# Optimization experiments

Hardware: AMD Instinct MI355X
Metric: run time of the kernel (lower is better)

## Reference

```python
import jax, jax.numpy as jnp
import numpy as np

TOKENS = 16384
DIM = 7168
N_EXPERTS = 256
N_GROUPS = 8          # n_expert_groups
TOPK_GROUPS = 4       # n_limited_groups
TOPK = 8              # n_activated_experts
ROUTE_SCALE = 2.5


def setup_inputs() -> dict:
    key = jax.random.key(0)
    k1, k2, k3 = jax.random.split(key, 3)
    x = jax.random.normal(k1, (TOKENS, DIM), dtype=jnp.float32)
    weight = jax.random.normal(k2, (N_EXPERTS, DIM), dtype=jnp.float32) * 0.02
    bias = jax.random.normal(k3, (N_EXPERTS,), dtype=jnp.float32) * 0.02
    return {"x": x, "weight": weight, "bias": bias}


def reference(x, weight, bias):
    T = x.shape[0]
    # router GEMM: [T, D] @ [D, E] -> [T, E]
    logits = jnp.einsum('td,ed->te', x, weight)
    scores = jax.nn.sigmoid(logits)            # score_func == 'sigmoid'
    original_scores = scores
    scores = scores + bias                     # bias path (dim == 7168)
    # group-limited routing: [T, G, E/G]
    sg = scores.reshape(T, N_GROUPS, -1)
    # bias is not None -> group score = sum of top-2 per group
    group_scores = jax.lax.top_k(sg, 2)[0].sum(axis=-1)          # [T, G]
    gidx = jax.lax.top_k(group_scores, TOPK_GROUPS)[1]           # [T, topk_groups]
    mask = jnp.zeros((T, N_GROUPS), dtype=scores.dtype)
    mask = mask.at[jnp.arange(T)[:, None], gidx].set(1.0)        # scatter mask
    scores_masked = (sg * mask[:, :, None]).reshape(T, -1)       # [T, E]
    idx = jax.lax.top_k(scores_masked, TOPK)[1]                  # [T, topk]
    w = jnp.take_along_axis(original_scores, idx, axis=1)        # gather
    w = w / w.sum(axis=-1, keepdims=True)                        # sigmoid norm
    w = w * ROUTE_SCALE
    return w.astype(x.dtype), idx
```

## Files before the change

### kernel.cpp

```cpp
#include <hip/hip_runtime.h>
#include <float.h>
#include <math.h>

#define TOKENS 16384
#define DIM    7168
#define NEXP   256
#define BM     32
#define BK     32
#define NCHUNK (DIM / BK)
#define ROUTE_SCALE 2.5
#define TAU      6e-6f
#define WSCALE   1024.0f
#define WUNSCALE 0.0009765625f
#define FIXCAP   8192

typedef _Float16 half8  __attribute__((ext_vector_type(8)));
typedef _Float16 half4v __attribute__((ext_vector_type(4)));
typedef float    f32x4  __attribute__((ext_vector_type(4)));

#define WPLANE 1835008

__device__ __forceinline__ _Float16 hi16(float f) { return (_Float16)f; }
__device__ __forceinline__ _Float16 lo16(float f) {
    _Float16 h = (_Float16)f;
    return (_Float16)(f - (float)h);
}

__global__ __launch_bounds__(256)
void conv_w(const float* __restrict__ W, _Float16* __restrict__ Wh, _Float16* __restrict__ Wl,
            int* __restrict__ cnt) {
    if (blockIdx.x == 0 && threadIdx.x == 0) *cnt = 0;
    int i = blockIdx.x * 256 + threadIdx.x;
    int f = i * 4;
    int e = f / DIM;
    int k = f - e * DIM;
    float4 v = ((const float4*)W)[i];
    v.x *= WSCALE; v.y *= WSCALE; v.z *= WSCALE; v.w *= WSCALE;
    half4v h, l;
    h[0] = hi16(v.x); l[0] = lo16(v.x);
    h[1] = hi16(v.y); l[1] = lo16(v.y);
    h[2] = hi16(v.z); l[2] = lo16(v.z);
    h[3] = hi16(v.w); l[3] = lo16(v.w);
    int o = ((k >> 5) << 13) + (e << 5) + (k & 31);
    *(half4v*)(Wh + o) = h;
    *(half4v*)(Wl + o) = l;
}

#define MFMA16(a, b, c) __builtin_amdgcn_mfma_f32_16x16x32_f16(a, b, c, 0, 0, 0)

#define VWAIT(n) do { \
    asm volatile("s_waitcnt vmcnt(" #n ")" ::: "memory"); \
    __builtin_amdgcn_sched_barrier(0); \
} while (0)

#define ISSUE_WS(c, S) do { \
    const _Float16* _p = wph0 + (size_t)(c) * 8192; \
    const _Float16* _q = wpl0 + (size_t)(c) * 8192; \
    asm volatile("global_load_dwordx4 %0, %1, off"             : "=&v"(S##h0) : "v"(_p)); \
    asm volatile("global_load_dwordx4 %0, %1, off offset:1024" : "=&v"(S##h1) : "v"(_p)); \
    asm volatile("global_load_dwordx4 %0, %1, off"             : "=&v"(S##l0) : "v"(_q)); \
    asm volatile("global_load_dwordx4 %0, %1, off offset:1024" : "=&v"(S##l1) : "v"(_q)); \
} while (0)

#define ISSUE_XP(gg, XA, XB) do { \
    const float* _px = xsrc + (size_t)(gg) * 64; \
    asm volatile("global_load_dwordx4 %0, %1, off"           : "=&v"(XA) : "v"(_px)); \
    asm volatile("global_load_dwordx4 %0, %1, off offset:16" : "=&v"(XB) : "v"(_px)); \
} while (0)

#define COMPUTE(ABP, BH0, BH1, BL0, BL1) do { \
    const _Float16* _ab = (ABP); \
    half8 ah0 = *(const half8*)(_ab + abase0); \
    half8 ah1 = *(const half8*)(_ab + abase1); \
    half8 al0 = *(const half8*)(_ab + 1024 + abase0); \
    half8 al1 = *(const half8*)(_ab + 1024 + abase1); \
    __builtin_amdgcn_s_setprio(1); \
    acc00 = MFMA16(ah0, BH0, acc00); acc00 = MFMA16(ah0, BL0, acc00); acc00 = MFMA16(al0, BH0, acc00); \
    acc01 = MFMA16(ah0, BH1, acc01); acc01 = MFMA16(ah0, BL1, acc01); acc01 = MFMA16(al0, BH1, acc01); \
    acc10 = MFMA16(ah1, BH0, acc10); acc10 = MFMA16(ah1, BL0, acc10); acc10 = MFMA16(al1, BH0, acc10); \
    acc11 = MFMA16(ah1, BH1, acc11); acc11 = MFMA16(ah1, BL1, acc11); acc11 = MFMA16(al1, BH1, acc11); \
    __builtin_amdgcn_s_setprio(0); \
} while (0)

#define COMPUTE_S(ABP, S) COMPUTE(ABP, S##h0, S##h1, S##l0, S##l1)

#define DUMPF() do { \
    accf00 += acc00; acc00 = (f32x4)(0.0f); \
    accf01 += acc01; acc01 = (f32x4)(0.0f); \
    accf10 += acc10; acc10 = (f32x4)(0.0f); \
    accf11 += acc11; acc11 = (f32x4)(0.0f); \
} while (0)

#define CONVERT_WRITE_XP(dstbuf, XA, XB) do { \
    half8 h8, l8; \
    const float v[8] = {XA.x, XA.y, XA.z, XA.w, XB.x, XB.y, XB.z, XB.w}; \
    _Pragma("unroll") \
    for (int e = 0; e < 8; ++e) { h8[e] = hi16(v[e]); l8[e] = lo16(v[e]); } \
    _Float16* d = hb + (dstbuf) * 4096 + xdst; \
    *(half8*)(d)        = h8; \
    *(half8*)(d + 1024) = l8; \
} while (0)

__global__ __launch_bounds__(256, 4)
void gate_main(const float* __restrict__ X, const _Float16* __restrict__ Wh,
               const _Float16* __restrict__ Wl, float* __restrict__ LG) {
    __shared__ _Float16 hb[8192];

    const int tid  = threadIdx.x;
    const int lane = tid & 63;
    const int ns   = tid >> 6;
    const int bid  = blockIdx.x;
    const int eh   = (bid >> 2) & 1;
    const int mt   = (bid >> 3) * 4 + (bid & 3);
    const int m0   = mt * BM;
    const int fr   = lane & 15;
    const int fk   = lane >> 4;

    const int xcc = tid >> 7;
    const int xr  = (tid >> 2) & 31;
    const int xs  = tid & 3;
    const float* xsrc = X + (size_t)(m0 + xr) * DIM + xcc * 32 + xs * 8;
    const int xdst = xcc * 2048 + xr * 32 + ((xs ^ ((xr >> 1) & 3)) << 3);

    const int row0 = fr;
    const int row1 = fr + 16;
    const int abase0 = row0 * 32 + ((fk ^ ((row0 >> 1) & 3)) << 3);
    const int abase1 = row1 * 32 + ((fk ^ ((row1 >> 1) & 3)) << 3);

    const int wro = ((eh * 128 + ns * 32 + fr) << 5) + fk * 8;
    const _Float16* wph0 = Wh + wro;
    const _Float16* wpl0 = Wl + wro;

    f32x4 acc00 = {}, acc01 = {}, acc10 = {}, acc11 = {};
    f32x4 accf00 = {}, accf01 = {}, accf10 = {}, accf11 = {};
    half8 S0h0, S0h1, S0l0, S0l1;
    half8 S1h0, S1h1, S1l0, S1l1;
    half8 S2h0, S2h1, S2l0, S2l1;
    half8 S3h0, S3h1, S3l0, S3l1;
    float4 xa, xb;
    float4 xc, xd;

    {
        float4 pa = *(const float4*)(xsrc);
        float4 pb = *(const float4*)(xsrc + 4);
        half8 h8, l8;
        const float v[8] = {pa.x, pa.y, pa.z, pa.w, pb.x, pb.y, pb.z, pb.w};
        #pragma unroll
        for (int e = 0; e < 8; ++e) { h8[e] = hi16(v[e]); l8[e] = lo16(v[e]); }
        *(half8*)(hb + xdst)        = h8;
        *(half8*)(hb + xdst + 1024) = l8;
    }
    asm volatile("s_waitcnt vmcnt(0) lgkmcnt(0)" ::: "memory");
    __builtin_amdgcn_sched_barrier(0);
    ISSUE_XP(1, xc, xd);
    ISSUE_WS(0, S0);
    ISSUE_WS(1, S1);
    __builtin_amdgcn_s_barrier();

    for (int k = 0; k < 55; ++k) {
        const int c4 = k * 4;
        VWAIT(4); ISSUE_XP(2 * k + 2, xa, xb); ISSUE_WS(c4 + 2, S2); COMPUTE_S(hb,        S0);
        VWAIT(6); ISSUE_WS(c4 + 3, S3);                              COMPUTE_S(hb + 2048, S1);
        CONVERT_WRITE_XP(1, xc, xd);
        asm volatile("s_waitcnt lgkmcnt(0)" ::: "memory");
        __builtin_amdgcn_s_barrier();
        VWAIT(4); ISSUE_XP(2 * k + 3, xc, xd); ISSUE_WS(c4 + 4, S0); COMPUTE_S(hb + 4096, S2);
        VWAIT(6); ISSUE_WS(c4 + 5, S1);                              COMPUTE_S(hb + 6144, S3);
        if ((k & 3) == 3) DUMPF();
        CONVERT_WRITE_XP(0, xa, xb);
        asm volatile("s_waitcnt lgkmcnt(0)" ::: "memory");
        __builtin_amdgcn_s_barrier();
    }
    VWAIT(4); ISSUE_WS(222, S2); COMPUTE_S(hb,        S0);
    VWAIT(4); ISSUE_WS(223, S3); COMPUTE_S(hb + 2048, S1);
    CONVERT_WRITE_XP(1, xc, xd);
    asm volatile("s_waitcnt lgkmcnt(0)" ::: "memory");
    __builtin_amdgcn_s_barrier();
    VWAIT(4); COMPUTE_S(hb + 4096, S2);
    VWAIT(0); COMPUTE_S(hb + 6144, S3);
    DUMPF();

    {
        f32x4 af[2][2] = {{accf00, accf01}, {accf10, accf11}};
        #pragma unroll
        for (int m = 0; m < 2; ++m)
            #pragma unroll
            for (int n = 0; n < 2; ++n)
                #pragma unroll
                for (int r = 0; r < 4; ++r) {
                    int t = m0 + m * 16 + fk * 4 + r;
                    int e = eh * 128 + ns * 32 + n * 16 + fr;
                    LG[(size_t)t * 256 + e] = af[m][n][r] * WUNSCALE;
                }
    }
}

__global__ __launch_bounds__(1024)
void gate_route(const float* __restrict__ LG, const float* __restrict__ Bp,
                float* __restrict__ outw, float* __restrict__ outi,
                int* __restrict__ cnt, int* __restrict__ list) {
    const int lane = threadIdx.x & 63;
    const int wv   = threadIdx.x >> 6;
    const int nw   = gridDim.x * 16;
    const int e0   = lane * 4;

    const float4 b4 = ((const float4*)Bp)[lane];

    for (int t = blockIdx.x * 16 + wv; t < TOKENS; t += nw) {
        float4 v4 = ((const float4*)LG)[(size_t)t * 64 + lane];
        const float s0 = 1.0f / (1.0f + expf(-v4.x));
        const float s1 = 1.0f / (1.0f + expf(-v4.y));
        const float s2 = 1.0f / (1.0f + expf(-v4.z));
        const float s3 = 1.0f / (1.0f + expf(-v4.w));
        const float c0 = s0 + b4.x, c1 = s1 + b4.y, c2 = s2 + b4.z, c3 = s3 + b4.w;

        float m1 = -FLT_MAX, m2 = -FLT_MAX;
        m2 = fmaxf(m2, fminf(m1, c0)); m1 = fmaxf(m1, c0);
        m2 = fmaxf(m2, fminf(m1, c1)); m1 = fmaxf(m1, c1);
        m2 = fmaxf(m2, fminf(m1, c2)); m1 = fmaxf(m1, c2);
        m2 = fmaxf(m2, fminf(m1, c3)); m1 = fmaxf(m1, c3);
        #pragma unroll
        for (int m = 1; m < 8; m <<= 1) {
            float o1 = __shfl_xor(m1, m);
            float o2 = __shfl_xor(m2, m);
            float hi = fmaxf(m1, o1);
            float lo = fmaxf(fminf(m1, o1), fmaxf(m2, o2));
            m1 = hi; m2 = lo;
        }
        const float gsl = m1 + m2;
        float gs[8];
        #pragma unroll
        for (int j = 0; j < 8; ++j) gs[j] = __shfl(gsl, j * 8);

        unsigned sel = 0;
        #pragma unroll
        for (int r = 0; r < 4; ++r) {
            float best = -FLT_MAX; int bg = 0;
            #pragma unroll
            for (int g = 0; g < 8; ++g) {
                int ok = (((sel >> g) & 1) == 0) & (gs[g] > best);
                best = ok ? gs[g] : best;
                bg   = ok ? g : bg;
            }
            sel |= 1u << bg;
        }
        float selmin = FLT_MAX, unselmax = -FLT_MAX;
        #pragma unroll
        for (int g = 0; g < 8; ++g) {
            int s = (sel >> g) & 1;
            selmin   = s ? fminf(selmin, gs[g])   : selmin;
            unselmax = s ? unselmax : fmaxf(unselmax, gs[g]);
        }
        bool flag = (selmin - unselmax) < (2.0f * TAU);

        const int gsel = (sel >> (lane >> 3)) & 1;
        const float z0 = gsel ? c0 : 0.0f;
        const float z1 = gsel ? c1 : 0.0f;
        const float z2 = gsel ? c2 : 0.0f;
        const float z3 = gsel ? c3 : 0.0f;

        float pv = FLT_MAX; int pe = -1;
        float wv8[8]; int ie8[8]; float wsum = 0.f;
        #pragma unroll
        for (int j = 0; j < 9; ++j) {
            float best = -FLT_MAX; int be = 0;
            {
                int af0 = (z0 < pv) | ((z0 == pv) & (e0     > pe));
                int tk0 = af0 & (z0 > best); best = tk0 ? z0 : best; be = tk0 ? e0     : be;
                int af1 = (z1 < pv) | ((z1 == pv) & (e0 + 1 > pe));
                int tk1 = af1 & (z1 > best); best = tk1 ? z1 : best; be = tk1 ? e0 + 1 : be;
                int af2 = (z2 < pv) | ((z2 == pv) & (e0 + 2 > pe));
                int tk2 = af2 & (z2 > best); best = tk2 ? z2 : best; be = tk2 ? e0 + 2 : be;
                int af3 = (z3 < pv) | ((z3 == pv) & (e0 + 3 > pe));
                int tk3 = af3 & (z3 > best); best = tk3 ? z3 : best; be = tk3 ? e0 + 3 : be;
            }
            #pragma unroll
            for (int m = 1; m < 64; m <<= 1) {
                float ov = __shfl_xor(best, m);
                int   oe = __shfl_xor(be, m);
                int take = (ov > best) | ((ov == best) & (oe < be));
                best = take ? ov : best;
                be   = take ? oe : be;
            }
            if (j > 0) flag = flag || ((pv - best) < TAU);
            if (j < 8) {
                const int ol = be >> 2, oi = be & 3;
                float w0 = __shfl(s0, ol), w1 = __shfl(s1, ol);
                float w2 = __shfl(s2, ol), w3 = __shfl(s3, ol);
                float ow = (oi == 0) ? w0 : (oi == 1) ? w1 : (oi == 2) ? w2 : w3;
                wv8[j] = ow; ie8[j] = be; wsum += ow;
            }
            pv = best; pe = be;
        }

        if (lane == 0) {
            if (flag) {
                int slot = atomicAdd(cnt, 1);
                list[slot] = t;
            }
            float scale = (float)ROUTE_SCALE / wsum;
            #pragma unroll
            for (int j = 0; j < 8; ++j) {
                outw[(size_t)t * 8 + j] = wv8[j] * scale;
                outi[(size_t)t * 8 + j] = (float)ie8[j];
            }
        }
    }
}

__global__ __launch_bounds__(256)
void gate_fix_dot(const float* __restrict__ X, const float* __restrict__ W,
                  const int* __restrict__ cnt, const int* __restrict__ list,
                  double* __restrict__ sig) {
    __shared__ float wlds[4 * DIM];
    const int tid  = threadIdx.x;
    const int lane = tid & 63;
    const int wv   = tid >> 6;
    const int eb   = blockIdx.x >> 2;
    const int tb   = blockIdx.x & 3;
    const int e    = eb * 4 + wv;
    int n = *cnt; if (n > FIXCAP) n = FIXCAP;

    for (int i = tid; i < DIM; i += 256)
        ((float4*)wlds)[i] = ((const float4*)(W + (size_t)eb * 4 * DIM))[i];
    __syncthreads();

    const float* wrow = wlds + wv * DIM;
    for (int li = tb; li < n; li += 8) {
        const int t0  = list[li];
        const int li1 = li + 4;
        const bool v1 = (li1 < n);
        const int t1  = v1 ? list[li1] : t0;
        const float* xr0 = X + (size_t)t0 * DIM;
        const float* xr1 = X + (size_t)t1 * DIM;
        double a0 = 0, a1 = 0, a2 = 0, a3 = 0;
        double b0 = 0, b1 = 0, b2 = 0, b3 = 0;
        for (int kk = 0; kk < DIM / 256; ++kk) {
            const int k = kk * 256 + lane * 4;
            float4 w4 = *(const float4*)(wrow + k);
            float4 x4 = *(const float4*)(xr0 + k);
            float4 y4 = *(const float4*)(xr1 + k);
            a0 = fma((double)x4.x, (double)w4.x, a0);
            a1 = fma((double)x4.y, (double)w4.y, a1);
            a2 = fma((double)x4.z, (double)w4.z, a2);
            a3 = fma((double)x4.w, (double)w4.w, a3);
            b0 = fma((double)y4.x, (double)w4.x, b0);
            b1 = fma((double)y4.y, (double)w4.y, b1);
            b2 = fma((double)y4.z, (double)w4.z, b2);
            b3 = fma((double)y4.w, (double)w4.w, b3);
        }
        double da = (a0 + a1) + (a2 + a3);
        double db = (b0 + b1) + (b2 + b3);
        #pragma unroll
        for (int m = 1; m < 64; m <<= 1) {
            da += __shfl_xor(da, m);
            db += __shfl_xor(db, m);
        }
        if (lane == 0) {
            sig[(size_t)li * 256 + e] = 1.0 / (1.0 + exp(-da));
            if (v1) sig[(size_t)li1 * 256 + e] = 1.0 / (1.0 + exp(-db));
        }
    }
}

__global__ __launch_bounds__(256)
void gate_fix_route(const float* __restrict__ Bp, float* __restrict__ outw,
                    float* __restrict__ outi, const int* __restrict__ cnt,
                    const int* __restrict__ list, const double* __restrict__ sig) {
    const int lane = threadIdx.x & 63;
    const int wv   = threadIdx.x >> 6;
    const int nw   = gridDim.x * 4;
    const int e0   = lane * 4;
    int n = *cnt; if (n > FIXCAP) n = FIXCAP;

    const float4 bf = ((const float4*)Bp)[lane];
    const double q0 = (double)bf.x, q1 = (double)bf.y, q2 = (double)bf.z, q3 = (double)bf.w;

    for (int li = blockIdx.x * 4 + wv; li < n; li += nw) {
        const int t = list[li];
        const double2 sa = ((const double2*)(sig + (size_t)li * 256))[lane * 2];
        const double2 sb = ((const double2*)(sig + (size_t)li * 256))[lane * 2 + 1];
        const double s0 = sa.x, s1 = sa.y, s2 = sb.x, s3 = sb.y;
        const double c0 = s0 + q0, c1 = s1 + q1, c2 = s2 + q2, c3 = s3 + q3;

        double m1 = -DBL_MAX, m2 = -DBL_MAX;
        m2 = fmax(m2, fmin(m1, c0)); m1 = fmax(m1, c0);
        m2 = fmax(m2, fmin(m1, c1)); m1 = fmax(m1, c1);
        m2 = fmax(m2, fmin(m1, c2)); m1 = fmax(m1, c2);
        m2 = fmax(m2, fmin(m1, c3)); m1 = fmax(m1, c3);
        #pragma unroll
        for (int m = 1; m < 8; m <<= 1) {
            double o1 = __shfl_xor(m1, m);
            double o2 = __shfl_xor(m2, m);
            double hi = fmax(m1, o1);
            double lo = fmax(fmin(m1, o1), fmax(m2, o2));
            m1 = hi; m2 = lo;
        }
        const double gsl = m1 + m2;
        double gs[8];
        #pragma unroll
        for (int j = 0; j < 8; ++j) gs[j] = __shfl(gsl, j * 8);

        unsigned sel = 0;
        #pragma unroll
        for (int r = 0; r < 4; ++r) {
            double best = -DBL_MAX; int bg = 0;
            #pragma unroll
            for (int g = 0; g < 8; ++g) {
                int ok = (((sel >> g) & 1) == 0) & (gs[g] > best);
                best = ok ? gs[g] : best;
                bg   = ok ? g : bg;
            }
            sel |= 1u << bg;
        }
        const int gsel = (sel >> (lane >> 3)) & 1;
        const double z0 = gsel ? c0 : 0.0;
        const double z1 = gsel ? c1 : 0.0;
        const double z2 = gsel ? c2 : 0.0;
        const double z3 = gsel ? c3 : 0.0;

        double pv = DBL_MAX; int pe = -1;
        double wv8[8]; int ie8[8]; double wsum = 0.0;
        #pragma unroll
        for (int j = 0; j < 8; ++j) {
            double best = -DBL_MAX; int be = 0;
            {
                int af0 = (z0 < pv) | ((z0 == pv) & (e0     > pe));
                int tk0 = af0 & (z0 > best); best = tk0 ? z0 : best; be = tk0 ? e0     : be;
                int af1 = (z1 < pv) | ((z1 == pv) & (e0 + 1 > pe));
                int tk1 = af1 & (z1 > best); best = tk1 ? z1 : best; be = tk1 ? e0 + 1 : be;
                int af2 = (z2 < pv) | ((z2 == pv) & (e0 + 2 > pe));
                int tk2 = af2 & (z2 > best); best = tk2 ? z2 : best; be = tk2 ? e0 + 2 : be;
                int af3 = (z3 < pv) | ((z3 == pv) & (e0 + 3 > pe));
                int tk3 = af3 & (z3 > best); best = tk3 ? z3 : best; be = tk3 ? e0 + 3 : be;
            }
            #pragma unroll
            for (int m = 1; m < 64; m <<= 1) {
                double ov = __shfl_xor(best, m);
                int    oe = __shfl_xor(be, m);
                int take = (ov > best) | ((ov == best) & (oe < be));
                best = take ? ov : best;
                be   = take ? oe : be;
            }
            {
                const int ol = be >> 2, oi = be & 3;
                double w0 = __shfl(s0, ol), w1 = __shfl(s1, ol);
                double w2 = __shfl(s2, ol), w3 = __shfl(s3, ol);
                double ow = (oi == 0) ? w0 : (oi == 1) ? w1 : (oi == 2) ? w2 : w3;
                wv8[j] = ow; ie8[j] = be; wsum += ow;
            }
            pv = best; pe = be;
        }
        if (lane == 0) {
            #pragma unroll
            for (int j = 0; j < 8; ++j) {
                outw[(size_t)t * 8 + j] = (float)((wv8[j] / wsum) * ROUTE_SCALE);
                outi[(size_t)t * 8 + j] = (float)ie8[j];
            }
        }
    }
}

extern "C" void kernel_launch(void* const* d_in, const int* in_sizes, int n_in,
                              void* d_out, int out_size, void* d_ws, size_t ws_size,
                              hipStream_t stream) {
    const float* X  = (const float*)d_in[0];
    const float* W  = (const float*)d_in[1];
    const float* Bp = (const float*)d_in[2];
    float* outw = (float*)d_out;
    float* outi = (float*)d_out + (size_t)TOKENS * 8;

    _Float16* Wh = (_Float16*)d_ws;
    _Float16* Wl = Wh + WPLANE;
    int* cnt  = (int*)(Wl + WPLANE);
    int* list = (int*)((char*)cnt + 16);
    float* LG = (float*)(list + TOKENS);
    double* sig = (double*)LG;

    conv_w        <<<dim3(WPLANE / 1024), dim3(256),  0, stream>>>(W, Wh, Wl, cnt);
    gate_main     <<<dim3(1024),          dim3(256),  0, stream>>>(X, Wh, Wl, LG);
    gate_route    <<<dim3(256),           dim3(1024), 0, stream>>>(LG, Bp, outw, outi, cnt, list);
    gate_fix_dot  <<<dim3(256),           dim3(256),  0, stream>>>(X, W, cnt, list, sig);
    gate_fix_route<<<dim3(64),            dim3(256),  0, stream>>>(Bp, outw, outi, cnt, list, sig);
}
```

Baseline: 454.2 us.

## Halve per-block expert tile to 64 and double grid for higher occupancy

Each block now computes a 32-token by 64-expert tile with one 16-wide expert fragment per wave, halving weight register staging and accumulators. The grid doubles to 2048 blocks and launch bounds target 6 waves per SIMD to improve latency hiding. In exchange, each token tile's X data is loaded and split into fp16 halves by four blocks instead of two. Each LDS A-fragment read now feeds half as many MFMAs.

```diff
diff --git a/kernel.cpp b/kernel.cpp
--- a/kernel.cpp
+++ b/kernel.cpp
@@ -53,13 +53,11 @@
     __builtin_amdgcn_sched_barrier(0); \
 } while (0)
 
-#define ISSUE_WS(c, S) do { \
+#define ISSUE_W2(c, H, L) do { \
     const _Float16* _p = wph0 + (size_t)(c) * 8192; \
     const _Float16* _q = wpl0 + (size_t)(c) * 8192; \
-    asm volatile("global_load_dwordx4 %0, %1, off"             : "=&v"(S##h0) : "v"(_p)); \
-    asm volatile("global_load_dwordx4 %0, %1, off offset:1024" : "=&v"(S##h1) : "v"(_p)); \
-    asm volatile("global_load_dwordx4 %0, %1, off"             : "=&v"(S##l0) : "v"(_q)); \
-    asm volatile("global_load_dwordx4 %0, %1, off offset:1024" : "=&v"(S##l1) : "v"(_q)); \
+    asm volatile("global_load_dwordx4 %0, %1, off" : "=&v"(H) : "v"(_p)); \
+    asm volatile("global_load_dwordx4 %0, %1, off" : "=&v"(L) : "v"(_q)); \
 } while (0)
 
 #define ISSUE_XP(gg, XA, XB) do { \
@@ -68,27 +66,21 @@
     asm volatile("global_load_dwordx4 %0, %1, off offset:16" : "=&v"(XB) : "v"(_px)); \
 } while (0)
 
-#define COMPUTE(ABP, BH0, BH1, BL0, BL1) do { \
+#define COMPUTE2(ABP, BH, BL) do { \
     const _Float16* _ab = (ABP); \
     half8 ah0 = *(const half8*)(_ab + abase0); \
     half8 ah1 = *(const half8*)(_ab + abase1); \
     half8 al0 = *(const half8*)(_ab + 1024 + abase0); \
     half8 al1 = *(const half8*)(_ab + 1024 + abase1); \
     __builtin_amdgcn_s_setprio(1); \
-    acc00 = MFMA16(ah0, BH0, acc00); acc00 = MFMA16(ah0, BL0, acc00); acc00 = MFMA16(al0, BH0, acc00); \
-    acc01 = MFMA16(ah0, BH1, acc01); acc01 = MFMA16(ah0, BL1, acc01); acc01 = MFMA16(al0, BH1, acc01); \
-    acc10 = MFMA16(ah1, BH0, acc10); acc10 = MFMA16(ah1, BL0, acc10); acc10 = MFMA16(al1, BH0, acc10); \
-    acc11 = MFMA16(ah1, BH1, acc11); acc11 = MFMA16(ah1, BL1, acc11); acc11 = MFMA16(al1, BH1, acc11); \
+    acc0 = MFMA16(ah0, BH, acc0); acc0 = MFMA16(ah0, BL, acc0); acc0 = MFMA16(al0, BH, acc0); \
+    acc1 = MFMA16(ah1, BH, acc1); acc1 = MFMA16(ah1, BL, acc1); acc1 = MFMA16(al1, BH, acc1); \
     __builtin_amdgcn_s_setprio(0); \
 } while (0)
 
-#define COMPUTE_S(ABP, S) COMPUTE(ABP, S##h0, S##h1, S##l0, S##l1)
-
 #define DUMPF() do { \
-    accf00 += acc00; acc00 = (f32x4)(0.0f); \
-    accf01 += acc01; acc01 = (f32x4)(0.0f); \
-    accf10 += acc10; acc10 = (f32x4)(0.0f); \
-    accf11 += acc11; acc11 = (f32x4)(0.0f); \
+    accf0 += acc0; acc0 = (f32x4)(0.0f); \
+    accf1 += acc1; acc1 = (f32x4)(0.0f); \
 } while (0)
 
 #define CONVERT_WRITE_XP(dstbuf, XA, XB) do { \
@@ -101,7 +93,7 @@
     *(half8*)(d + 1024) = l8; \
 } while (0)
 
-__global__ __launch_bounds__(256, 4)
+__global__ __launch_bounds__(256, 6)
 void gate_main(const float* __restrict__ X, const _Float16* __restrict__ Wh,
                const _Float16* __restrict__ Wl, float* __restrict__ LG) {
     __shared__ _Float16 hb[8192];
@@ -110,8 +102,8 @@
     const int lane = tid & 63;
     const int ns   = tid >> 6;
     const int bid  = blockIdx.x;
-    const int eh   = (bid >> 2) & 1;
-    const int mt   = (bid >> 3) * 4 + (bid & 3);
+    const int eq   = (bid >> 1) & 3;
+    const int mt   = (bid >> 3) * 2 + (bid & 1);
     const int m0   = mt * BM;
     const int fr   = lane & 15;
     const int fk   = lane >> 4;
@@ -127,16 +119,13 @@
     const int abase0 = row0 * 32 + ((fk ^ ((row0 >> 1) & 3)) << 3);
     const int abase1 = row1 * 32 + ((fk ^ ((row1 >> 1) & 3)) << 3);
 
-    const int wro = ((eh * 128 + ns * 32 + fr) << 5) + fk * 8;
+    const int wro = ((eq * 64 + ns * 16 + fr) << 5) + fk * 8;
     const _Float16* wph0 = Wh + wro;
     const _Float16* wpl0 = Wl + wro;
 
-    f32x4 acc00 = {}, acc01 = {}, acc10 = {}, acc11 = {};
-    f32x4 accf00 = {}, accf01 = {}, accf10 = {}, accf11 = {};
-    half8 S0h0, S0h1, S0l0, S0l1;
-    half8 S1h0, S1h1, S1l0, S1l1;
-    half8 S2h0, S2h1, S2l0, S2l1;
-    half8 S3h0, S3h1, S3l0, S3l1;
+    f32x4 acc0 = {}, acc1 = {};
+    f32x4 accf0 = {}, accf1 = {};
+    half8 S0h, S0l, S1h, S1l, S2h, S2l, S3h, S3l;
     float4 xa, xb;
     float4 xc, xd;
 
@@ -153,45 +142,43 @@
     asm volatile("s_waitcnt vmcnt(0) lgkmcnt(0)" ::: "memory");
     __builtin_amdgcn_sched_barrier(0);
     ISSUE_XP(1, xc, xd);
-    ISSUE_WS(0, S0);
-    ISSUE_WS(1, S1);
+    ISSUE_W2(0, S0h, S0l);
+    ISSUE_W2(1, S1h, S1l);
     __builtin_amdgcn_s_barrier();
 
     for (int k = 0; k < 55; ++k) {
         const int c4 = k * 4;
-        VWAIT(4); ISSUE_XP(2 * k + 2, xa, xb); ISSUE_WS(c4 + 2, S2); COMPUTE_S(hb,        S0);
-        VWAIT(6); ISSUE_WS(c4 + 3, S3);                              COMPUTE_S(hb + 2048, S1);
+        VWAIT(2); ISSUE_XP(2 * k + 2, xa, xb); ISSUE_W2(c4 + 2, S2h, S2l); COMPUTE2(hb,        S0h, S0l);
+        VWAIT(4); ISSUE_W2(c4 + 3, S3h, S3l);                              COMPUTE2(hb + 2048, S1h, S1l);
         CONVERT_WRITE_XP(1, xc, xd);
         asm volatile("s_waitcnt lgkmcnt(0)" ::: "memory");
         __builtin_amdgcn_s_barrier();
-        VWAIT(4); ISSUE_XP(2 * k + 3, xc, xd); ISSUE_WS(c4 + 4, S0); COMPUTE_S(hb + 4096, S2);
-        VWAIT(6); ISSUE_WS(c4 + 5, S1);                              COMPUTE_S(hb + 6144, S3);
+        VWAIT(2); ISSUE_XP(2 * k + 3, xc, xd); ISSUE_W2(c4 + 4, S0h, S0l); COMPUTE2(hb + 4096, S2h, S2l);
+        VWAIT(4); ISSUE_W2(c4 + 5, S1h, S1l);                              COMPUTE2(hb + 6144, S3h, S3l);
         if ((k & 3) == 3) DUMPF();
         CONVERT_WRITE_XP(0, xa, xb);
         asm volatile("s_waitcnt lgkmcnt(0)" ::: "memory");
         __builtin_amdgcn_s_barrier();
     }
-    VWAIT(4); ISSUE_WS(222, S2); COMPUTE_S(hb,        S0);
-    VWAIT(4); ISSUE_WS(223, S3); COMPUTE_S(hb + 2048, S1);
+    VWAIT(2); ISSUE_W2(222, S2h, S2l); COMPUTE2(hb,        S0h, S0l);
+    VWAIT(2); ISSUE_W2(223, S3h, S3l); COMPUTE2(hb + 2048, S1h, S1l);
     CONVERT_WRITE_XP(1, xc, xd);
     asm volatile("s_waitcnt lgkmcnt(0)" ::: "memory");
     __builtin_amdgcn_s_barrier();
-    VWAIT(4); COMPUTE_S(hb + 4096, S2);
-    VWAIT(0); COMPUTE_S(hb + 6144, S3);
+    VWAIT(2); COMPUTE2(hb + 4096, S2h, S2l);
+    VWAIT(0); COMPUTE2(hb + 6144, S3h, S3l);
     DUMPF();
 
     {
-        f32x4 af[2][2] = {{accf00, accf01}, {accf10, accf11}};
+        f32x4 af[2] = {accf0, accf1};
         #pragma unroll
         for (int m = 0; m < 2; ++m)
             #pragma unroll
-            for (int n = 0; n < 2; ++n)
-                #pragma unroll
-                for (int r = 0; r < 4; ++r) {
-                    int t = m0 + m * 16 + fk * 4 + r;
-                    int e = eh * 128 + ns * 32 + n * 16 + fr;
-                    LG[(size_t)t * 256 + e] = af[m][n][r] * WUNSCALE;
-                }
+            for (int r = 0; r < 4; ++r) {
+                int t = m0 + m * 16 + fk * 4 + r;
+                int e = eq * 64 + ns * 16 + fr;
+                LG[(size_t)t * 256 + e] = af[m][r] * WUNSCALE;
+            }
     }
 }
 
@@ -478,7 +465,7 @@
     double* sig = (double*)LG;
 
     conv_w        <<<dim3(WPLANE / 1024), dim3(256),  0, stream>>>(W, Wh, Wl, cnt);
-    gate_main     <<<dim3(1024),          dim3(256),  0, stream>>>(X, Wh, Wl, LG);
+    gate_main     <<<dim3(2048),          dim3(256),  0, stream>>>(X, Wh, Wl, LG);
     gate_route    <<<dim3(256),           dim3(1024), 0, stream>>>(LG, Bp, outw, outi, cnt, list);
     gate_fix_dot  <<<dim3(256),           dim3(256),  0, stream>>>(X, W, cnt, list, sig);
     gate_fix_route<<<dim3(64),            dim3(256),  0, stream>>>(Bp, outw, outi, cnt, list, sig);
```

Measured after the change: 577.8 us. +27.2%, slower.
